# Kernel tuning notes

Hardware: AMD Instinct MI355X
Metric: run time of the kernel (lower is better)

## Reference

```python
import jax, jax.numpy as jnp
import numpy as np
import math

D = 1024      # d_model
H = 16        # nhead
HD = D // H   # head_dim
FF = 4096     # dim_feedforward
NE = 4        # encoder layers
ND = 4        # decoder layers
S = 1024      # src len
T = 1024      # tgt len
B = 2         # batch
EPS = 1e-5


def _ln(x, g, b):
    m = jnp.mean(x, axis=-1, keepdims=True)
    v = jnp.mean((x - m) ** 2, axis=-1, keepdims=True)
    return (x - m) / jnp.sqrt(v + EPS) * g + b


def _mha(xq, xkv, Wq, Wk, Wv, Wo, bo):
    # xq: [T, B, D], xkv: [S, B, D]
    Tl, Bb, _ = xq.shape
    Sl = xkv.shape[0]
    q = (xq @ Wq.T).reshape(Tl, Bb * H, HD).transpose(1, 0, 2) / math.sqrt(HD)
    k = (xkv @ Wk.T).reshape(Sl, Bb * H, HD).transpose(1, 0, 2)
    v = (xkv @ Wv.T).reshape(Sl, Bb * H, HD).transpose(1, 0, 2)
    attn = jax.nn.softmax(jnp.einsum('zte,zse->zts', q, k), axis=-1)  # [B*H, T, S]
    o = jnp.einsum('zts,zse->zte', attn, v)                            # [B*H, T, HD]
    o = o.transpose(1, 0, 2).reshape(Tl, Bb, D)
    return o @ Wo.T + bo


def _ffn(x, W1, b1, W2, b2):
    return jax.nn.relu(x @ W1.T + b1) @ W2.T + b2


def _forward(src, tgt,
             enc_Wq, enc_Wk, enc_Wv, enc_Wo, enc_bo,
             enc_ln1_g, enc_ln1_b, enc_W1, enc_b1, enc_W2, enc_b2,
             enc_ln2_g, enc_ln2_b, enc_fn_g, enc_fn_b,
             dec_sWq, dec_sWk, dec_sWv, dec_sWo, dec_sbo,
             dec_ln1_g, dec_ln1_b,
             dec_cWq, dec_cWk, dec_cWv, dec_cWo, dec_cbo,
             dec_ln2_g, dec_ln2_b,
             dec_W1, dec_b1, dec_W2, dec_b2,
             dec_ln3_g, dec_ln3_b, dec_fn_g, dec_fn_b):
    # Encoder (post-norm)
    x = src
    for i in range(NE):
        x = _ln(x + _mha(x, x, enc_Wq[i], enc_Wk[i], enc_Wv[i], enc_Wo[i], enc_bo[i]),
                enc_ln1_g[i], enc_ln1_b[i])
        x = _ln(x + _ffn(x, enc_W1[i], enc_b1[i], enc_W2[i], enc_b2[i]),
                enc_ln2_g[i], enc_ln2_b[i])
    memory = _ln(x, enc_fn_g, enc_fn_b)
    # Decoder (post-norm): self-attn, cross-attn, FFN
    y = tgt
    for i in range(ND):
        y = _ln(y + _mha(y, y, dec_sWq[i], dec_sWk[i], dec_sWv[i], dec_sWo[i], dec_sbo[i]),
                dec_ln1_g[i], dec_ln1_b[i])
        y = _ln(y + _mha(y, memory, dec_cWq[i], dec_cWk[i], dec_cWv[i], dec_cWo[i], dec_cbo[i]),
                dec_ln2_g[i], dec_ln2_b[i])
        y = _ln(y + _ffn(y, dec_W1[i], dec_b1[i], dec_W2[i], dec_b2[i]),
                dec_ln3_g[i], dec_ln3_b[i])
    return _ln(y, dec_fn_g, dec_fn_b)


def setup_inputs() -> dict:
    key = jax.random.key(0)
    ks = iter(jax.random.split(key, 128))

    def w(shape, scale=0.02):
        return jax.random.normal(next(ks), shape, dtype=jnp.float32) * scale

    inp = {}
    inp['src'] = jax.random.normal(next(ks), (S, B, D), dtype=jnp.float32)
    inp['tgt'] = jax.random.normal(next(ks), (T, B, D), dtype=jnp.float32)
    # encoder
    inp['enc_Wq'] = w((NE, D, D)); inp['enc_Wk'] = w((NE, D, D)); inp['enc_Wv'] = w((NE, D, D))
    inp['enc_Wo'] = w((NE, D, D)); inp['enc_bo'] = jnp.zeros((NE, D), jnp.float32)
    inp['enc_ln1_g'] = jnp.ones((NE, D), jnp.float32); inp['enc_ln1_b'] = jnp.zeros((NE, D), jnp.float32)
    inp['enc_W1'] = w((NE, FF, D)); inp['enc_b1'] = jnp.zeros((NE, FF), jnp.float32)
    inp['enc_W2'] = w((NE, D, FF)); inp['enc_b2'] = jnp.zeros((NE, D), jnp.float32)
    inp['enc_ln2_g'] = jnp.ones((NE, D), jnp.float32); inp['enc_ln2_b'] = jnp.zeros((NE, D), jnp.float32)
    inp['enc_fn_g'] = jnp.ones((D,), jnp.float32); inp['enc_fn_b'] = jnp.zeros((D,), jnp.float32)
    # decoder
    inp['dec_sWq'] = w((ND, D, D)); inp['dec_sWk'] = w((ND, D, D)); inp['dec_sWv'] = w((ND, D, D))
    inp['dec_sWo'] = w((ND, D, D)); inp['dec_sbo'] = jnp.zeros((ND, D), jnp.float32)
    inp['dec_ln1_g'] = jnp.ones((ND, D), jnp.float32); inp['dec_ln1_b'] = jnp.zeros((ND, D), jnp.float32)
    inp['dec_cWq'] = w((ND, D, D)); inp['dec_cWk'] = w((ND, D, D)); inp['dec_cWv'] = w((ND, D, D))
    inp['dec_cWo'] = w((ND, D, D)); inp['dec_cbo'] = jnp.zeros((ND, D), jnp.float32)
    inp['dec_ln2_g'] = jnp.ones((ND, D), jnp.float32); inp['dec_ln2_b'] = jnp.zeros((ND, D), jnp.float32)
    inp['dec_W1'] = w((ND, FF, D)); inp['dec_b1'] = jnp.zeros((ND, FF), jnp.float32)
    inp['dec_W2'] = w((ND, D, FF)); inp['dec_b2'] = jnp.zeros((ND, D), jnp.float32)
    inp['dec_ln3_g'] = jnp.ones((ND, D), jnp.float32); inp['dec_ln3_b'] = jnp.zeros((ND, D), jnp.float32)
    inp['dec_fn_g'] = jnp.ones((D,), jnp.float32); inp['dec_fn_b'] = jnp.zeros((D,), jnp.float32)
    return inp


def reference(src, tgt,
              enc_Wq, enc_Wk, enc_Wv, enc_Wo, enc_bo,
              enc_ln1_g, enc_ln1_b, enc_W1, enc_b1, enc_W2, enc_b2,
              enc_ln2_g, enc_ln2_b, enc_fn_g, enc_fn_b,
              dec_sWq, dec_sWk, dec_sWv, dec_sWo, dec_sbo,
              dec_ln1_g, dec_ln1_b,
              dec_cWq, dec_cWk, dec_cWv, dec_cWo, dec_cbo,
              dec_ln2_g, dec_ln2_b,
              dec_W1, dec_b1, dec_W2, dec_b2,
              dec_ln3_g, dec_ln3_b, dec_fn_g, dec_fn_b):
    return _forward(src, tgt,
                    enc_Wq, enc_Wk, enc_Wv, enc_Wo, enc_bo,
                    enc_ln1_g, enc_ln1_b, enc_W1, enc_b1, enc_W2, enc_b2,
                    enc_ln2_g, enc_ln2_b, enc_fn_g, enc_fn_b,
                    dec_sWq, dec_sWk, dec_sWv, dec_sWo, dec_sbo,
                    dec_ln1_g, dec_ln1_b,
                    dec_cWq, dec_cWk, dec_cWv, dec_cWo, dec_cbo,
                    dec_ln2_g, dec_ln2_b,
                    dec_W1, dec_b1, dec_W2, dec_b2,
                    dec_ln3_g, dec_ln3_b, dec_fn_g, dec_fn_b)
```

## Files before the change

kernel.cpp:

```cpp
#include <hip/hip_runtime.h>

#define DI __device__ __forceinline__

typedef __attribute__((ext_vector_type(4))) float f32x4;
typedef __attribute__((ext_vector_type(8))) short short8;
typedef __attribute__((ext_vector_type(4))) short s16x4;
typedef unsigned short u16;
typedef unsigned long long u64;

#define GLDS(gp, lp)                                              \
  __builtin_amdgcn_global_load_lds(                               \
      (const __attribute__((address_space(1))) void*)(gp),        \
      (__attribute__((address_space(3))) void*)(lp), 16, 0, 0)

DI u16 f2bf(float f) {
  unsigned u = __builtin_bit_cast(unsigned, f);
  u += 0x7fffu + ((u >> 16) & 1u);
  return (u16)(u >> 16);
}
DI float bf2f(u16 h) {
  unsigned u = ((unsigned)h) << 16;
  return __builtin_bit_cast(float, u);
}

template <int MODE>
__global__ __launch_bounds__(256, 2) void gemm_bt(
    const u16* __restrict__ Ap, const u16* __restrict__ Ap2,
    const u16* __restrict__ Bp, void* __restrict__ Cp, void* __restrict__ Cp2,
    void* __restrict__ Cp3, const float* __restrict__ bias, int N, int lda,
    int ldb, int kz, int NT, long sB, long sC, float scale) {
  constexpr int BM = 128, BN = 128;
  constexpr int WM = BM / 2, WN = BN / 2, FM = WM / 16, FN = WN / 16;
  constexpr int ATILE = BM * 128, TILE = ATILE + BN * 128;

  __shared__ char smem[2 * TILE];

  const int tid = threadIdx.x;
  const int wid = tid >> 6, lane = tid & 63;
  const int z = blockIdx.z;
  const long bm = (long)blockIdx.y * BM;
  const long bn = (long)blockIdx.x * BN;
  const int kofs = z * kz;

  const u16* A16 = (MODE == 2 && z > 0) ? Ap2 : Ap;
  const u16* B16 = Bp + (long)z * sB;

  const int lrow = lane >> 3;
  const int lslot = (lane & 7) ^ lrow;
  const u16* asrc0 = A16 + (bm + lrow) * (long)lda + kofs + lslot * 8;
  const u16* bsrc0 = B16 + (bn + lrow) * (long)ldb + kofs + lslot * 8;

  auto stage = [&](int kt, char* buf) {
    const u16* as = asrc0 + kt * 64;
    const u16* bs = bsrc0 + kt * 64;
#pragma unroll
    for (int c = 0; c < 4; c++) {
      int chunk = wid * 4 + c;
      GLDS(as + (long)chunk * 8 * lda, buf + chunk * 1024);
    }
#pragma unroll
    for (int c = 0; c < 4; c++) {
      int chunk = wid * 4 + c;
      GLDS(bs + (long)chunk * 8 * ldb, buf + ATILE + chunk * 1024);
    }
  };

  const int wm = wid >> 1, wn = wid & 1;
  const int l15 = lane & 15, ks = lane >> 4;

  f32x4 acc[FM][FN];
#pragma unroll
  for (int i = 0; i < FM; i++)
#pragma unroll
    for (int j = 0; j < FN; j++) acc[i][j] = (f32x4){0.f, 0.f, 0.f, 0.f};

  auto compute = [&](const char* buf) {
    const char* As = buf;
    const char* Bs = buf + ATILE;
#pragma unroll
    for (int kk = 0; kk < 2; kk++) {
      short8 af[FM], bfr[FN];
#pragma unroll
      for (int i = 0; i < FM; i++) {
        int row = wm * WM + i * 16 + l15;
        int byte = row * 128 + kk * 64 + ks * 16;
        byte ^= (row & 7) << 4;
        af[i] = *(const short8*)(As + byte);
      }
#pragma unroll
      for (int j = 0; j < FN; j++) {
        int row = wn * WN + j * 16 + l15;
        int byte = row * 128 + kk * 64 + ks * 16;
        byte ^= (row & 7) << 4;
        bfr[j] = *(const short8*)(Bs + byte);
      }
#pragma unroll
      for (int i = 0; i < FM; i++)
#pragma unroll
        for (int j = 0; j < FN; j++)
          acc[i][j] = __builtin_amdgcn_mfma_f32_16x16x32_bf16(af[i], bfr[j],
                                                              acc[i][j], 0, 0, 0);
    }
  };

  stage(0, smem);
  __syncthreads();
  for (int t = 0; t < NT; ++t) {
    char* cur = smem + (t & 1) * TILE;
    char* nxt = smem + ((t + 1) & 1) * TILE;
    if (t + 1 < NT) stage(t + 1, nxt);
    compute(cur);
    __syncthreads();
  }

  const float scl = (MODE == 2 && z > 0) ? 1.f : scale;
#pragma unroll
  for (int i = 0; i < FM; i++) {
#pragma unroll
    for (int j = 0; j < FN; j++) {
#pragma unroll
      for (int r = 0; r < 4; r++) {
        long m = bm + wm * WM + i * 16 + ks * 4 + r;
        long n = bn + wn * WN + j * 16 + l15;
        float val = acc[i][j][r] * scl;
        if constexpr (MODE == 0) {
          ((float*)Cp)[z * sC + m * (long)N + n] = val;
        } else if constexpr (MODE == 1) {
          val += bias[n];
          ((u16*)Cp)[m * (long)N + n] = f2bf(fmaxf(val, 0.f));
        } else if constexpr (MODE == 2) {
          u16* Cz = (u16*)(z == 0 ? Cp : (z == 1 ? Cp2 : Cp3));
          long t_ = m >> 1;
          int b_ = (int)(m & 1), h_ = (int)(n >> 6), d_ = (int)(n & 63);
          Cz[(((long)(b_ * 16 + h_) * 1024 + t_) << 6) + d_] = f2bf(val);
        }
      }
    }
  }
}

__global__ __launch_bounds__(256) void castw_k(const float* __restrict__ a,
                                               const float* __restrict__ b,
                                               const float* __restrict__ c,
                                               const float* __restrict__ d,
                                               u16* __restrict__ out,
                                               long per) {
  const int y = blockIdx.y;
  const float* s = y == 0 ? a : (y == 1 ? b : (y == 2 ? c : d));
  const long i = ((long)blockIdx.x * 256 + threadIdx.x) * 4;
  f32x4 v = *(const f32x4*)(s + i);
  s16x4 hh;
#pragma unroll
  for (int j = 0; j < 4; j++) hh[j] = (short)f2bf(v[j]);
  *(s16x4*)(out + y * per + i) = hh;
}

__global__ __launch_bounds__(256) void transpose_v_k(const u16* __restrict__ v,
                                                     u16* __restrict__ vt) {
  __shared__ u16 tile[64][68];
  const int z = blockIdx.y;
  const int t0 = blockIdx.x * 64;
  const int tid = threadIdx.x;
  const int r = tid >> 2, c0 = (tid & 3) * 16;
  const u16* src = v + ((long)z * 1024 + t0 + r) * 64 + c0;
  short8 v0 = *(const short8*)src;
  short8 v1 = *(const short8*)(src + 8);
#pragma unroll
  for (int j = 0; j < 8; j++) {
    tile[r][c0 + j] = (u16)v0[j];
    tile[r][c0 + 8 + j] = (u16)v1[j];
  }
  __syncthreads();
  short8 o0, o1;
#pragma unroll
  for (int j = 0; j < 8; j++) {
    o0[j] = (short)tile[c0 + j][r];
    o1[j] = (short)tile[c0 + 8 + j][r];
  }
  u16* dst = vt + ((long)z * 64 + r) * 1024 + t0 + c0;
  *(short8*)dst = o0;
  *(short8*)(dst + 8) = o1;
}

__global__ __launch_bounds__(256, 2) void flash_k(
    const u16* __restrict__ q, const u16* __restrict__ kb,
    const u16* __restrict__ vt, u16* __restrict__ ab) {
  __shared__ char Ks[2][8192];
  __shared__ char Vs[2][8192];
  __shared__ char P_lds[4][2048];
  __shared__ float stats[4][16];

  const int tid = threadIdx.x;
  const int wid = tid >> 6, lane = tid & 63;
  const int l15 = lane & 15, ks = lane >> 4;
  const int z = blockIdx.y;
  const int q0 = blockIdx.x * 64 + wid * 16;

  const u16* Qz = q + (long)z * 65536;
  const u16* Kz = kb + (long)z * 65536;
  const u16* Vz = vt + (long)z * 65536;
  char* Pw = P_lds[wid];
  float* st = stats[wid];

  const int r_l = lane >> 3;
  const int swsl = ((lane & 7) ^ r_l) * 8;

  auto stageKV = [&](int t, int buf) {
    const int kv0 = t * 64;
#pragma unroll
    for (int c = 0; c < 2; c++) {
      int chunk = wid * 2 + c;
      GLDS(Kz + (long)(kv0 + chunk * 8 + r_l) * 64 + swsl,
           Ks[buf] + chunk * 1024);
      GLDS(Vz + (long)(chunk * 8 + r_l) * 1024 + kv0 + swsl,
           Vs[buf] + chunk * 1024);
    }
  };

  short8 qf[2];
#pragma unroll
  for (int kk = 0; kk < 2; kk++)
    qf[kk] = *(const short8*)(Qz + (q0 + l15) * 64 + kk * 32 + ks * 8);

  f32x4 Oacc[4];
#pragma unroll
  for (int nf = 0; nf < 4; nf++) Oacc[nf] = (f32x4){0.f, 0.f, 0.f, 0.f};
  float mrun = -1e30f, lrun = 0.f;

  stageKV(0, 0);
  __syncthreads();
  for (int t = 0; t < 16; ++t) {
    const int cur = t & 1;
    if (t + 1 < 16) stageKV(t + 1, cur ^ 1);
    f32x4 s[4];
#pragma unroll
    for (int m = 0; m < 4; m++) s[m] = (f32x4){0.f, 0.f, 0.f, 0.f};
#pragma unroll
    for (int kk = 0; kk < 2; kk++) {
#pragma unroll
      for (int m = 0; m < 4; m++) {
        int row = m * 16 + l15;
        int byte = row * 128 + kk * 64 + ks * 16;
        byte ^= (row & 7) << 4;
        short8 kf = *(const short8*)(Ks[cur] + byte);
        s[m] = __builtin_amdgcn_mfma_f32_16x16x32_bf16(kf, qf[kk], s[m], 0, 0, 0);
      }
    }
    float tmax = s[0][0];
#pragma unroll
    for (int m = 0; m < 4; m++)
#pragma unroll
      for (int r = 0; r < 4; r++) tmax = fmaxf(tmax, s[m][r]);
    tmax = fmaxf(tmax, __shfl_xor(tmax, 16));
    tmax = fmaxf(tmax, __shfl_xor(tmax, 32));
    const float mnew = fmaxf(mrun, tmax);
    const float factor = __expf(mrun - mnew);
    float psum = 0.f;
#pragma unroll
    for (int m = 0; m < 4; m++) {
      u16 p4[4];
#pragma unroll
      for (int r = 0; r < 4; r++) {
        float e = __expf(s[m][r] - mnew);
        psum += e;
        p4[r] = f2bf(e);
      }
      u64 pk = (u64)p4[0] | ((u64)p4[1] << 16) | ((u64)p4[2] << 32) |
               ((u64)p4[3] << 48);
      int byte = l15 * 128 + m * 32 + ks * 8;
      byte ^= (l15 & 7) << 4;
      *(u64*)(Pw + byte) = pk;
    }
    psum += __shfl_xor(psum, 16);
    psum += __shfl_xor(psum, 32);
    lrun = lrun * factor + psum;
    mrun = mnew;
    if (ks == 0) st[l15] = factor;
    f32x4 facv = *(const f32x4*)&st[ks * 4];
#pragma unroll
    for (int nf = 0; nf < 4; nf++)
#pragma unroll
      for (int r = 0; r < 4; r++) Oacc[nf][r] *= facv[r];
#pragma unroll
    for (int kk = 0; kk < 2; kk++) {
      int pb = l15 * 128 + kk * 64 + ks * 16;
      pb ^= (l15 & 7) << 4;
      short8 pa = *(const short8*)(Pw + pb);
#pragma unroll
      for (int nf = 0; nf < 4; nf++) {
        int row = nf * 16 + l15;
        int vb_ = row * 128 + kk * 64 + ks * 16;
        vb_ ^= (row & 7) << 4;
        short8 vf = *(const short8*)(Vs[cur] + vb_);
        Oacc[nf] = __builtin_amdgcn_mfma_f32_16x16x32_bf16(pa, vf, Oacc[nf],
                                                           0, 0, 0);
      }
    }
    __syncthreads();
  }
  if (ks == 0) st[l15] = 1.f / lrun;
  f32x4 invv = *(const f32x4*)&st[ks * 4];
  const int b_ = z >> 4, h_ = z & 15;
#pragma unroll
  for (int nf = 0; nf < 4; nf++) {
#pragma unroll
    for (int r = 0; r < 4; r++) {
      int qg = q0 + ks * 4 + r;
      ab[((long)(qg * 2 + b_) << 10) + h_ * 64 + nf * 16 + l15] =
          f2bf(Oacc[nf][r] * invv[r]);
    }
  }
}

template <int NP>
__global__ __launch_bounds__(256) void add_ln_k(
    const float* __restrict__ x, const float* __restrict__ parts,
    const float* __restrict__ cb, const float* __restrict__ g,
    const float* __restrict__ b, float* __restrict__ out,
    u16* __restrict__ outh) {
  const long row = blockIdx.x;
  const int tid = threadIdx.x;
  const long base = row * 1024 + tid * 4;
  f32x4 v = *(const f32x4*)(x + base);
#pragma unroll
  for (int p = 0; p < NP; p++) {
    f32x4 q = *(const f32x4*)(parts + (long)p * 2048 * 1024 + base);
    v[0] += q[0]; v[1] += q[1]; v[2] += q[2]; v[3] += q[3];
  }
  if (cb) {
    f32x4 q = *(const f32x4*)(cb + tid * 4);
    v[0] += q[0]; v[1] += q[1]; v[2] += q[2]; v[3] += q[3];
  }
  float s = v[0] + v[1] + v[2] + v[3];
  float s2 = v[0] * v[0] + v[1] * v[1] + v[2] * v[2] + v[3] * v[3];
#pragma unroll
  for (int off = 1; off < 64; off <<= 1) {
    s += __shfl_xor(s, off);
    s2 += __shfl_xor(s2, off);
  }
  __shared__ float ps[8];
  const int wid = tid >> 6, lane = tid & 63;
  if (lane == 0) {
    ps[wid] = s;
    ps[4 + wid] = s2;
  }
  __syncthreads();
  s = ps[0] + ps[1] + ps[2] + ps[3];
  s2 = ps[4] + ps[5] + ps[6] + ps[7];
  float mean = s * (1.f / 1024.f);
  float var = s2 * (1.f / 1024.f) - mean * mean;
  float rstd = rsqrtf(var + 1e-5f);
  f32x4 gg = *(const f32x4*)(g + tid * 4);
  f32x4 bb = *(const f32x4*)(b + tid * 4);
  f32x4 o;
#pragma unroll
  for (int j = 0; j < 4; j++) o[j] = (v[j] - mean) * rstd * gg[j] + bb[j];
  *(f32x4*)(out + base) = o;
  if (outh) {
    s16x4 hh;
#pragma unroll
    for (int j = 0; j < 4; j++) hh[j] = (short)f2bf(o[j]);
    *(s16x4*)(outh + base) = hh;
  }
}

__global__ __launch_bounds__(256) void cast_k(const float* __restrict__ in,
                                              float* __restrict__ o32,
                                              u16* __restrict__ o16) {
  const long i = ((long)blockIdx.x * 256 + threadIdx.x) * 4;
  f32x4 v = *(const f32x4*)(in + i);
  *(f32x4*)(o32 + i) = v;
  s16x4 hh;
#pragma unroll
  for (int j = 0; j < 4; j++) hh[j] = (short)f2bf(v[j]);
  *(s16x4*)(o16 + i) = hh;
}

extern "C" void kernel_launch(void* const* d_in, const int* in_sizes, int n_in,
                              void* d_out, int out_size, void* d_ws,
                              size_t ws_size, hipStream_t stream) {
  const float* src = (const float*)d_in[0];
  const float* tgt = (const float*)d_in[1];
  const float* enc_Wq = (const float*)d_in[2];
  const float* enc_Wk = (const float*)d_in[3];
  const float* enc_Wv = (const float*)d_in[4];
  const float* enc_Wo = (const float*)d_in[5];
  const float* enc_bo = (const float*)d_in[6];
  const float* enc_ln1_g = (const float*)d_in[7];
  const float* enc_ln1_b = (const float*)d_in[8];
  const float* enc_W1 = (const float*)d_in[9];
  const float* enc_b1 = (const float*)d_in[10];
  const float* enc_W2 = (const float*)d_in[11];
  const float* enc_b2 = (const float*)d_in[12];
  const float* enc_ln2_g = (const float*)d_in[13];
  const float* enc_ln2_b = (const float*)d_in[14];
  const float* enc_fn_g = (const float*)d_in[15];
  const float* enc_fn_b = (const float*)d_in[16];
  const float* dec_sWq = (const float*)d_in[17];
  const float* dec_sWk = (const float*)d_in[18];
  const float* dec_sWv = (const float*)d_in[19];
  const float* dec_sWo = (const float*)d_in[20];
  const float* dec_sbo = (const float*)d_in[21];
  const float* dec_ln1_g = (const float*)d_in[22];
  const float* dec_ln1_b = (const float*)d_in[23];
  const float* dec_cWq = (const float*)d_in[24];
  const float* dec_cWk = (const float*)d_in[25];
  const float* dec_cWv = (const float*)d_in[26];
  const float* dec_cWo = (const float*)d_in[27];
  const float* dec_cbo = (const float*)d_in[28];
  const float* dec_ln2_g = (const float*)d_in[29];
  const float* dec_ln2_b = (const float*)d_in[30];
  const float* dec_W1 = (const float*)d_in[31];
  const float* dec_b1 = (const float*)d_in[32];
  const float* dec_W2 = (const float*)d_in[33];
  const float* dec_b2 = (const float*)d_in[34];
  const float* dec_ln3_g = (const float*)d_in[35];
  const float* dec_ln3_b = (const float*)d_in[36];
  const float* dec_fn_g = (const float*)d_in[37];
  const float* dec_fn_b = (const float*)d_in[38];

  char* ws = (char*)d_ws;
  size_t off = 0;
  auto alloc = [&](size_t bytes) {
    void* p = ws + off;
    off += (bytes + 255) & ~(size_t)255;
    return p;
  };
  float* xf = (float*)alloc(2048L * 1024 * 4);
  float* mem = (float*)alloc(2048L * 1024 * 4);
  u16* xh = (u16*)alloc(2048L * 1024 * 2);
  u16* memh = (u16*)alloc(2048L * 1024 * 2);
  u16* h = (u16*)alloc(2048L * 4096 * 2);
  u16* q = (u16*)alloc(2048L * 1024 * 2);
  u16* kb = (u16*)alloc(2048L * 1024 * 2);
  u16* vb = (u16*)alloc(2048L * 1024 * 2);
  u16* vt = (u16*)alloc(2048L * 1024 * 2);
  u16* ab = (u16*)alloc(2048L * 1024 * 2);
  float* parts = (float*)alloc(4L * 2048 * 1024 * 4);
  u16* wbuf = (u16*)alloc(8L * 1024 * 1024 * 2);
  u16* wbig = (u16*)alloc(112L * 1024 * 1024 * 2);
  const bool mega = off <= ws_size;

  const long sP = 2048L * 1024;
  const long M1 = 1024L * 1024, M4 = 4L * 1024 * 1024;
  u16* encA = wbig;
  u16* encF = wbig + 16 * M1;
  u16* decS = wbig + 48 * M1;
  u16* decC = wbig + 64 * M1;
  u16* decF = wbig + 80 * M1;

  if (mega) {
    castw_k<<<dim3(4096, 4), 256, 0, stream>>>(enc_Wq, enc_Wk, enc_Wv, enc_Wo,
                                               encA, 4 * M1);
    castw_k<<<dim3(16384, 2), 256, 0, stream>>>(enc_W1, enc_W2, enc_W1, enc_W1,
                                                encF, 16 * M1);
    castw_k<<<dim3(4096, 4), 256, 0, stream>>>(dec_sWq, dec_sWk, dec_sWv,
                                               dec_sWo, decS, 4 * M1);
    castw_k<<<dim3(4096, 4), 256, 0, stream>>>(dec_cWq, dec_cWk, dec_cWv,
                                               dec_cWo, decC, 4 * M1);
    castw_k<<<dim3(16384, 2), 256, 0, stream>>>(dec_W1, dec_W2, dec_W1, dec_W1,
                                                decF, 16 * M1);
  }

  auto attn = [&](const u16* qin, const u16* kvin, const float* Wq,
                  const float* Wk, const float* Wv, const float* Wo,
                  const u16* bqkv, long sBq, const u16* bo) {
    if (!mega) {
      castw_k<<<dim3(1024, 4), 256, 0, stream>>>(Wq, Wk, Wv, Wo, wbuf, M1);
      bqkv = wbuf; sBq = M1; bo = wbuf + 3 * M1;
    }
    gemm_bt<2><<<dim3(8, 16, 3), 256, 0, stream>>>(
        qin, kvin, bqkv, q, kb, vb, nullptr,
        1024, 1024, 1024, 0, 16, sBq, 0, 0.125f);
    transpose_v_k<<<dim3(16, 32), 256, 0, stream>>>(vb, vt);
    flash_k<<<dim3(16, 32), 256, 0, stream>>>(q, kb, vt, ab);
    gemm_bt<0><<<dim3(8, 16, 2), 256, 0, stream>>>(
        ab, nullptr, bo, parts, nullptr, nullptr, nullptr,
        1024, 1024, 1024, 512, 8, 0, sP, 1.f);
  };
  auto ffn = [&](const u16* xin, const float* W1, const float* b1,
                 const float* W2, const u16* bw1, const u16* bw2) {
    if (!mega) {
      castw_k<<<dim3(4096, 2), 256, 0, stream>>>(W1, W2, W1, W1, wbuf, M4);
      bw1 = wbuf; bw2 = wbuf + M4;
    }
    gemm_bt<1><<<dim3(32, 16, 1), 256, 0, stream>>>(
        xin, nullptr, bw1, h, nullptr, nullptr, b1,
        4096, 1024, 1024, 0, 16, 0, 0, 1.f);
    gemm_bt<0><<<dim3(8, 16, 4), 256, 0, stream>>>(
        h, nullptr, bw2, parts, nullptr, nullptr, nullptr,
        1024, 4096, 4096, 1024, 16, 0, sP, 1.f);
  };

  const long DD = 1024L * 1024, Dv = 1024, FFD = 4096L * 1024, FFv = 4096;

  cast_k<<<dim3(2048), 256, 0, stream>>>(src, xf, xh);
  for (int i = 0; i < 4; i++) {
    attn(xh, xh, enc_Wq + i * DD, enc_Wk + i * DD, enc_Wv + i * DD,
         enc_Wo + i * DD, encA + i * M1, 4 * M1, encA + 12 * M1 + i * M1);
    add_ln_k<2><<<dim3(2048), 256, 0, stream>>>(
        xf, parts, enc_bo + i * Dv, enc_ln1_g + i * Dv, enc_ln1_b + i * Dv,
        xf, xh);
    ffn(xh, enc_W1 + i * FFD, enc_b1 + i * FFv, enc_W2 + i * FFD,
        encF + i * M4, encF + 16 * M1 + i * M4);
    add_ln_k<4><<<dim3(2048), 256, 0, stream>>>(
        xf, parts, enc_b2 + i * Dv, enc_ln2_g + i * Dv, enc_ln2_b + i * Dv,
        xf, xh);
  }
  add_ln_k<0><<<dim3(2048), 256, 0, stream>>>(
      xf, nullptr, nullptr, enc_fn_g, enc_fn_b, mem, memh);

  cast_k<<<dim3(2048), 256, 0, stream>>>(tgt, xf, xh);
  for (int i = 0; i < 4; i++) {
    attn(xh, xh, dec_sWq + i * DD, dec_sWk + i * DD, dec_sWv + i * DD,
         dec_sWo + i * DD, decS + i * M1, 4 * M1, decS + 12 * M1 + i * M1);
    add_ln_k<2><<<dim3(2048), 256, 0, stream>>>(
        xf, parts, dec_sbo + i * Dv, dec_ln1_g + i * Dv, dec_ln1_b + i * Dv,
        xf, xh);
    attn(xh, memh, dec_cWq + i * DD, dec_cWk + i * DD, dec_cWv + i * DD,
         dec_cWo + i * DD, decC + i * M1, 4 * M1, decC + 12 * M1 + i * M1);
    add_ln_k<2><<<dim3(2048), 256, 0, stream>>>(
        xf, parts, dec_cbo + i * Dv, dec_ln2_g + i * Dv, dec_ln2_b + i * Dv,
        xf, xh);
    ffn(xh, dec_W1 + i * FFD, dec_b1 + i * FFv, dec_W2 + i * FFD,
        decF + i * M4, decF + 16 * M1 + i * M4);
    add_ln_k<4><<<dim3(2048), 256, 0, stream>>>(
        xf, parts, dec_b2 + i * Dv, dec_ln3_g + i * Dv, dec_ln3_b + i * Dv,
        xf, xh);
  }
  add_ln_k<0><<<dim3(2048), 256, 0, stream>>>(
      xf, nullptr, nullptr, dec_fn_g, dec_fn_b, (float*)d_out, nullptr);
}
```

Measured before the change: 1.498 ms.

## Fuse fp32 weight cast into GEMM B loads and V transpose into QKV epilogue

The GEMM now reads fp32 weights directly, converts them to bf16 in registers with packed convert instructions and writes them into the swizzled LDS tile. This removes the separate weight-cast kernels and the large bf16 weight workspace. The V projection writes its output already transposed through an LDS staging tile, so the separate transpose kernel and its buffer go away. In exchange each GEMM reads twice the weight bytes and holds more registers for the B prefetch, and redoes the conversion once per M-tile row of blocks.

```diff
diff --git a/kernel.cpp b/kernel.cpp
--- a/kernel.cpp
+++ b/kernel.cpp
@@ -5,6 +5,7 @@
 typedef __attribute__((ext_vector_type(4))) float f32x4;
 typedef __attribute__((ext_vector_type(8))) short short8;
 typedef __attribute__((ext_vector_type(4))) short s16x4;
+typedef __attribute__((ext_vector_type(4))) unsigned u32x4;
 typedef unsigned short u16;
 typedef unsigned long long u64;
 
@@ -22,13 +23,20 @@
   unsigned u = ((unsigned)h) << 16;
   return __builtin_bit_cast(float, u);
 }
+DI unsigned cvtpk(float lo, float hi) {
+  unsigned r;
+  asm("v_cvt_pk_bf16_f32 %0, %1, %2" : "=v"(r) : "v"(lo), "v"(hi));
+  return r;
+}
 
 template <int MODE>
 __global__ __launch_bounds__(256, 2) void gemm_bt(
     const u16* __restrict__ Ap, const u16* __restrict__ Ap2,
-    const u16* __restrict__ Bp, void* __restrict__ Cp, void* __restrict__ Cp2,
-    void* __restrict__ Cp3, const float* __restrict__ bias, int N, int lda,
-    int ldb, int kz, int NT, long sB, long sC, float scale) {
+    const float* __restrict__ Bp, const float* __restrict__ Bp2,
+    const float* __restrict__ Bp3, void* __restrict__ Cp,
+    void* __restrict__ Cp2, void* __restrict__ Cp3,
+    const float* __restrict__ bias, int N, int lda, int ldb, int kz, int NT,
+    long sC, float scale) {
   constexpr int BM = 128, BN = 128;
   constexpr int WM = BM / 2, WN = BN / 2, FM = WM / 16, FN = WN / 16;
   constexpr int ATILE = BM * 128, TILE = ATILE + BN * 128;
@@ -43,25 +51,45 @@
   const int kofs = z * kz;
 
   const u16* A16 = (MODE == 2 && z > 0) ? Ap2 : Ap;
-  const u16* B16 = Bp + (long)z * sB;
+  const float* Bw = (MODE == 2) ? (z == 0 ? Bp : (z == 1 ? Bp2 : Bp3)) : Bp;
 
   const int lrow = lane >> 3;
   const int lslot = (lane & 7) ^ lrow;
   const u16* asrc0 = A16 + (bm + lrow) * (long)lda + kofs + lslot * 8;
-  const u16* bsrc0 = B16 + (bn + lrow) * (long)ldb + kofs + lslot * 8;
-
-  auto stage = [&](int kt, char* buf) {
+
+  auto stageA = [&](int kt, char* buf) {
     const u16* as = asrc0 + kt * 64;
-    const u16* bs = bsrc0 + kt * 64;
 #pragma unroll
     for (int c = 0; c < 4; c++) {
       int chunk = wid * 4 + c;
       GLDS(as + (long)chunk * 8 * lda, buf + chunk * 1024);
     }
+  };
+
+  const int rowB = tid >> 1, colB = (tid & 1) * 32;
+  const float* bsrc0 = Bw + (bn + rowB) * (long)ldb + kofs + colB;
+  float fb[32];
+
+  auto loadB = [&](int kt) {
+    const float* p = bsrc0 + kt * 64;
+#pragma unroll
+    for (int i = 0; i < 8; i++) {
+      f32x4 v = *(const f32x4*)(p + i * 4);
+#pragma unroll
+      for (int e = 0; e < 4; e++) fb[i * 4 + e] = v[e];
+    }
+  };
+  auto writeB = [&](char* buf) {
+    char* Bs = buf + ATILE;
 #pragma unroll
     for (int c = 0; c < 4; c++) {
-      int chunk = wid * 4 + c;
-      GLDS(bs + (long)chunk * 8 * ldb, buf + ATILE + chunk * 1024);
+      u32x4 w;
+#pragma unroll
+      for (int e = 0; e < 4; e++)
+        w[e] = cvtpk(fb[c * 8 + e * 2], fb[c * 8 + e * 2 + 1]);
+      int byte = rowB * 128 + (colB + c * 8) * 2;
+      byte ^= (rowB & 7) << 4;
+      *(u32x4*)(Bs + byte) = w;
     }
   };
 
@@ -103,14 +131,53 @@
     }
   };
 
-  stage(0, smem);
+  loadB(0);
+  stageA(0, smem);
+  writeB(smem);
   __syncthreads();
   for (int t = 0; t < NT; ++t) {
     char* cur = smem + (t & 1) * TILE;
     char* nxt = smem + ((t + 1) & 1) * TILE;
-    if (t + 1 < NT) stage(t + 1, nxt);
+    if (t + 1 < NT) { loadB(t + 1); stageA(t + 1, nxt); }
     compute(cur);
+    if (t + 1 < NT) writeB(nxt);
     __syncthreads();
+  }
+
+  if constexpr (MODE == 2) {
+    if (z == 2) {
+      char* tb = smem;
+#pragma unroll
+      for (int i = 0; i < FM; i++) {
+#pragma unroll
+        for (int j = 0; j < FN; j++) {
+          int np = wn * 64 + j * 16 + l15;
+          int basem = wm * 64 + i * 16 + ks * 4;
+          unsigned lo = (unsigned)f2bf(acc[i][j][0]) |
+                        ((unsigned)f2bf(acc[i][j][2]) << 16);
+          unsigned hi = (unsigned)f2bf(acc[i][j][1]) |
+                        ((unsigned)f2bf(acc[i][j][3]) << 16);
+          int byte0 = np * 256 + basem;
+          int byte1 = np * 256 + 128 + basem;
+          byte0 ^= (np & 7) << 4;
+          byte1 ^= (np & 7) << 4;
+          *(unsigned*)(tb + byte0) = lo;
+          *(unsigned*)(tb + byte1) = hi;
+        }
+      }
+      __syncthreads();
+      const int np = tid >> 1, bsel = tid & 1;
+      const int h_ = (int)((bn + np) >> 6), d_ = (int)((bn + np) & 63);
+      u16* dst = (u16*)Cp3 + ((long)(bsel * 16 + h_) * 64 + d_) * 1024 +
+                 (bm >> 1);
+#pragma unroll
+      for (int c = 0; c < 8; c++) {
+        int byte = np * 256 + bsel * 128 + c * 16;
+        byte ^= (np & 7) << 4;
+        *(short8*)(dst + c * 8) = *(const short8*)(tb + byte);
+      }
+      return;
+    }
   }
 
   const float scl = (MODE == 2 && z > 0) ? 1.f : scale;
@@ -129,7 +196,7 @@
           val += bias[n];
           ((u16*)Cp)[m * (long)N + n] = f2bf(fmaxf(val, 0.f));
         } else if constexpr (MODE == 2) {
-          u16* Cz = (u16*)(z == 0 ? Cp : (z == 1 ? Cp2 : Cp3));
+          u16* Cz = (u16*)(z == 0 ? Cp : Cp2);
           long t_ = m >> 1;
           int b_ = (int)(m & 1), h_ = (int)(n >> 6), d_ = (int)(n & 63);
           Cz[(((long)(b_ * 16 + h_) * 1024 + t_) << 6) + d_] = f2bf(val);
@@ -137,49 +204,6 @@
       }
     }
   }
-}
-
-__global__ __launch_bounds__(256) void castw_k(const float* __restrict__ a,
-                                               const float* __restrict__ b,
-                                               const float* __restrict__ c,
-                                               const float* __restrict__ d,
-                                               u16* __restrict__ out,
-                                               long per) {
-  const int y = blockIdx.y;
-  const float* s = y == 0 ? a : (y == 1 ? b : (y == 2 ? c : d));
-  const long i = ((long)blockIdx.x * 256 + threadIdx.x) * 4;
-  f32x4 v = *(const f32x4*)(s + i);
-  s16x4 hh;
-#pragma unroll
-  for (int j = 0; j < 4; j++) hh[j] = (short)f2bf(v[j]);
-  *(s16x4*)(out + y * per + i) = hh;
-}
-
-__global__ __launch_bounds__(256) void transpose_v_k(const u16* __restrict__ v,
-                                                     u16* __restrict__ vt) {
-  __shared__ u16 tile[64][68];
-  const int z = blockIdx.y;
-  const int t0 = blockIdx.x * 64;
-  const int tid = threadIdx.x;
-  const int r = tid >> 2, c0 = (tid & 3) * 16;
-  const u16* src = v + ((long)z * 1024 + t0 + r) * 64 + c0;
-  short8 v0 = *(const short8*)src;
-  short8 v1 = *(const short8*)(src + 8);
-#pragma unroll
-  for (int j = 0; j < 8; j++) {
-    tile[r][c0 + j] = (u16)v0[j];
-    tile[r][c0 + 8 + j] = (u16)v1[j];
-  }
-  __syncthreads();
-  short8 o0, o1;
-#pragma unroll
-  for (int j = 0; j < 8; j++) {
-    o0[j] = (short)tile[c0 + j][r];
-    o1[j] = (short)tile[c0 + 8 + j][r];
-  }
-  u16* dst = vt + ((long)z * 64 + r) * 1024 + t0 + c0;
-  *(short8*)dst = o0;
-  *(short8*)(dst + 8) = o1;
 }
 
 __global__ __launch_bounds__(256, 2) void flash_k(
@@ -433,63 +457,30 @@
   u16* h = (u16*)alloc(2048L * 4096 * 2);
   u16* q = (u16*)alloc(2048L * 1024 * 2);
   u16* kb = (u16*)alloc(2048L * 1024 * 2);
-  u16* vb = (u16*)alloc(2048L * 1024 * 2);
   u16* vt = (u16*)alloc(2048L * 1024 * 2);
   u16* ab = (u16*)alloc(2048L * 1024 * 2);
   float* parts = (float*)alloc(4L * 2048 * 1024 * 4);
-  u16* wbuf = (u16*)alloc(8L * 1024 * 1024 * 2);
-  u16* wbig = (u16*)alloc(112L * 1024 * 1024 * 2);
-  const bool mega = off <= ws_size;
 
   const long sP = 2048L * 1024;
-  const long M1 = 1024L * 1024, M4 = 4L * 1024 * 1024;
-  u16* encA = wbig;
-  u16* encF = wbig + 16 * M1;
-  u16* decS = wbig + 48 * M1;
-  u16* decC = wbig + 64 * M1;
-  u16* decF = wbig + 80 * M1;
-
-  if (mega) {
-    castw_k<<<dim3(4096, 4), 256, 0, stream>>>(enc_Wq, enc_Wk, enc_Wv, enc_Wo,
-                                               encA, 4 * M1);
-    castw_k<<<dim3(16384, 2), 256, 0, stream>>>(enc_W1, enc_W2, enc_W1, enc_W1,
-                                                encF, 16 * M1);
-    castw_k<<<dim3(4096, 4), 256, 0, stream>>>(dec_sWq, dec_sWk, dec_sWv,
-                                               dec_sWo, decS, 4 * M1);
-    castw_k<<<dim3(4096, 4), 256, 0, stream>>>(dec_cWq, dec_cWk, dec_cWv,
-                                               dec_cWo, decC, 4 * M1);
-    castw_k<<<dim3(16384, 2), 256, 0, stream>>>(dec_W1, dec_W2, dec_W1, dec_W1,
-                                                decF, 16 * M1);
-  }
 
   auto attn = [&](const u16* qin, const u16* kvin, const float* Wq,
-                  const float* Wk, const float* Wv, const float* Wo,
-                  const u16* bqkv, long sBq, const u16* bo) {
-    if (!mega) {
-      castw_k<<<dim3(1024, 4), 256, 0, stream>>>(Wq, Wk, Wv, Wo, wbuf, M1);
-      bqkv = wbuf; sBq = M1; bo = wbuf + 3 * M1;
-    }
+                  const float* Wk, const float* Wv, const float* Wo) {
     gemm_bt<2><<<dim3(8, 16, 3), 256, 0, stream>>>(
-        qin, kvin, bqkv, q, kb, vb, nullptr,
-        1024, 1024, 1024, 0, 16, sBq, 0, 0.125f);
-    transpose_v_k<<<dim3(16, 32), 256, 0, stream>>>(vb, vt);
+        qin, kvin, Wq, Wk, Wv, q, kb, vt, nullptr,
+        1024, 1024, 1024, 0, 16, 0, 0.125f);
     flash_k<<<dim3(16, 32), 256, 0, stream>>>(q, kb, vt, ab);
     gemm_bt<0><<<dim3(8, 16, 2), 256, 0, stream>>>(
-        ab, nullptr, bo, parts, nullptr, nullptr, nullptr,
-        1024, 1024, 1024, 512, 8, 0, sP, 1.f);
+        ab, nullptr, Wo, nullptr, nullptr, parts, nullptr, nullptr, nullptr,
+        1024, 1024, 1024, 512, 8, sP, 1.f);
   };
   auto ffn = [&](const u16* xin, const float* W1, const float* b1,
-                 const float* W2, const u16* bw1, const u16* bw2) {
-    if (!mega) {
-      castw_k<<<dim3(4096, 2), 256, 0, stream>>>(W1, W2, W1, W1, wbuf, M4);
-      bw1 = wbuf; bw2 = wbuf + M4;
-    }
+                 const float* W2) {
     gemm_bt<1><<<dim3(32, 16, 1), 256, 0, stream>>>(
-        xin, nullptr, bw1, h, nullptr, nullptr, b1,
-        4096, 1024, 1024, 0, 16, 0, 0, 1.f);
+        xin, nullptr, W1, nullptr, nullptr, h, nullptr, nullptr, b1,
+        4096, 1024, 1024, 0, 16, 0, 1.f);
     gemm_bt<0><<<dim3(8, 16, 4), 256, 0, stream>>>(
-        h, nullptr, bw2, parts, nullptr, nullptr, nullptr,
-        1024, 4096, 4096, 1024, 16, 0, sP, 1.f);
+        h, nullptr, W2, nullptr, nullptr, parts, nullptr, nullptr, nullptr,
+        1024, 4096, 4096, 1024, 16, sP, 1.f);
   };
 
   const long DD = 1024L * 1024, Dv = 1024, FFD = 4096L * 1024, FFv = 4096;
@@ -497,12 +488,11 @@
   cast_k<<<dim3(2048), 256, 0, stream>>>(src, xf, xh);
   for (int i = 0; i < 4; i++) {
     attn(xh, xh, enc_Wq + i * DD, enc_Wk + i * DD, enc_Wv + i * DD,
-         enc_Wo + i * DD, encA + i * M1, 4 * M1, encA + 12 * M1 + i * M1);
+         enc_Wo + i * DD);
     add_ln_k<2><<<dim3(2048), 256, 0, stream>>>(
         xf, parts, enc_bo + i * Dv, enc_ln1_g + i * Dv, enc_ln1_b + i * Dv,
         xf, xh);
-    ffn(xh, enc_W1 + i * FFD, enc_b1 + i * FFv, enc_W2 + i * FFD,
-        encF + i * M4, encF + 16 * M1 + i * M4);
+    ffn(xh, enc_W1 + i * FFD, enc_b1 + i * FFv, enc_W2 + i * FFD);
     add_ln_k<4><<<dim3(2048), 256, 0, stream>>>(
         xf, parts, enc_b2 + i * Dv, enc_ln2_g + i * Dv, enc_ln2_b + i * Dv,
         xf, xh);
@@ -513,17 +503,16 @@
   cast_k<<<dim3(2048), 256, 0, stream>>>(tgt, xf, xh);
   for (int i = 0; i < 4; i++) {
     attn(xh, xh, dec_sWq + i * DD, dec_sWk + i * DD, dec_sWv + i * DD,
-         dec_sWo + i * DD, decS + i * M1, 4 * M1, decS + 12 * M1 + i * M1);
+         dec_sWo + i * DD);
     add_ln_k<2><<<dim3(2048), 256, 0, stream>>>(
         xf, parts, dec_sbo + i * Dv, dec_ln1_g + i * Dv, dec_ln1_b + i * Dv,
         xf, xh);
     attn(xh, memh, dec_cWq + i * DD, dec_cWk + i * DD, dec_cWv + i * DD,
-         dec_cWo + i * DD, decC + i * M1, 4 * M1, decC + 12 * M1 + i * M1);
+         dec_cWo + i * DD);
     add_ln_k<2><<<dim3(2048), 256, 0, stream>>>(
         xf, parts, dec_cbo + i * Dv, dec_ln2_g + i * Dv, dec_ln2_b + i * Dv,
         xf, xh);
-    ffn(xh, dec_W1 + i * FFD, dec_b1 + i * FFv, dec_W2 + i * FFD,
-        decF + i * M4, decF + 16 * M1 + i * M4);
+    ffn(xh, dec_W1 + i * FFD, dec_b1 + i * FFv, dec_W2 + i * FFD);
     add_ln_k<4><<<dim3(2048), 256, 0, stream>>>(
         xf, parts, dec_b2 + i * Dv, dec_ln3_g + i * Dv, dec_ln3_b + i * Dv,
         xf, xh);
```

Measured after the change: 2.215 ms. +47.8%, slower.
